# Kernel tuning notes

Measured on AMD Instinct MI355X. Metric: run time of the kernel, lower is better.

Reference implementation:

```python
import jax, jax.numpy as jnp
import numpy as np

DIM = 384
HEADS = 12
WS = (2, 7, 7)
SS = (1, 3, 3)
B, D, H, W = 4, 8, 56, 56
N = WS[0] * WS[1] * WS[2]  # 98


def _win_part_np(x, ws):
    b, d, h, w, c = x.shape
    x = x.reshape(b, d // ws[0], ws[0], h // ws[1], ws[1], w // ws[2], ws[2], c)
    return x.transpose(0, 1, 3, 5, 2, 4, 6, 7).reshape(-1, ws[0] * ws[1] * ws[2], c)


def setup_inputs() -> dict:
    key = jax.random.key(0)
    ks = jax.random.split(key, 6)
    s = 0.02
    x = jax.random.normal(ks[0], (B, D, H, W, DIM), jnp.float32)
    # relative position index (static int buffer)
    coords = np.stack(np.meshgrid(np.arange(WS[0]), np.arange(WS[1]), np.arange(WS[2]), indexing='ij')).reshape(3, -1)
    rel = (coords[:, :, None] - coords[:, None, :]).transpose(1, 2, 0)
    rel[..., 0] += WS[0] - 1
    rel[..., 1] += WS[1] - 1
    rel[..., 2] += WS[2] - 1
    rel[..., 0] *= (2 * WS[1] - 1) * (2 * WS[2] - 1)
    rel[..., 1] *= 2 * WS[2] - 1
    rel_index = jnp.asarray(rel.sum(-1), jnp.int32)  # [N, N]
    # shifted-window attention mask (standard Swin construction)
    img = np.zeros((1, D, H, W, 1), np.float32)
    cnt = 0
    for dsl in (slice(0, -WS[0]), slice(-WS[0], -SS[0]), slice(-SS[0], None)):
        for hsl in (slice(0, -WS[1]), slice(-WS[1], -SS[1]), slice(-SS[1], None)):
            for wsl in (slice(0, -WS[2]), slice(-WS[2], -SS[2]), slice(-SS[2], None)):
                img[:, dsl, hsl, wsl, :] = cnt
                cnt += 1
    mw = _win_part_np(img, WS).squeeze(-1)  # [nW, N]
    attn_mask = np.where(mw[:, None, :] != mw[:, :, None], -100.0, 0.0).astype(np.float32)
    table_size = (2 * WS[0] - 1) * (2 * WS[1] - 1) * (2 * WS[2] - 1)
    return {
        'x': x,
        'mask': jnp.asarray(attn_mask),
        'rel_table': jax.random.normal(ks[1], (table_size, HEADS), jnp.float32) * s,
        'rel_index': rel_index,
        'qkv_w': jax.random.normal(ks[2], (3 * DIM, DIM), jnp.float32) * s,
        'qkv_b': jnp.zeros((3 * DIM,), jnp.float32),
        'proj_w': jax.random.normal(ks[3], (DIM, DIM), jnp.float32) * s,
        'proj_b': jnp.zeros((DIM,), jnp.float32),
        'g1': jnp.ones((DIM,), jnp.float32), 'b1': jnp.zeros((DIM,), jnp.float32),
        'g2': jnp.ones((DIM,), jnp.float32), 'b2': jnp.zeros((DIM,), jnp.float32),
        'fc1_w': jax.random.normal(ks[4], (DIM, DIM), jnp.float32) * s,
        'fc1_b': jnp.zeros((DIM,), jnp.float32),
        'fc2_w': jax.random.normal(ks[5], (DIM, DIM), jnp.float32) * s,
        'fc2_b': jnp.zeros((DIM,), jnp.float32),
    }


def _ln(x, g, b, eps=1e-5):
    mu = x.mean(-1, keepdims=True)
    var = jnp.mean((x - mu) ** 2, axis=-1, keepdims=True)
    return (x - mu) * jax.lax.rsqrt(var + eps) * g + b


def _window_partition(x, ws):
    b, d, h, w, c = x.shape
    x = x.reshape(b, d // ws[0], ws[0], h // ws[1], ws[1], w // ws[2], ws[2], c)
    return x.transpose(0, 1, 3, 5, 2, 4, 6, 7).reshape(-1, ws[0] * ws[1] * ws[2], c)


def _window_reverse(win, ws, b, d, h, w):
    x = win.reshape(b, d // ws[0], h // ws[1], w // ws[2], ws[0], ws[1], ws[2], -1)
    return x.transpose(0, 1, 4, 2, 5, 3, 6, 7).reshape(b, d, h, w, -1)


def reference(x, mask, rel_table, rel_index, qkv_w, qkv_b, proj_w, proj_b,
              g1, b1, g2, b2, fc1_w, fc1_b, fc2_w, fc2_b):
    shortcut = x
    h = _ln(x, g1, b1)
    b, d, hh, ww, c = h.shape
    # get_window_size: clamp window/shift to input extents (static here)
    ws = [min(WS[i], (d, hh, ww)[i]) for i in range(3)]
    ss = [0 if (d, hh, ww)[i] <= WS[i] else SS[i] for i in range(3)]
    pad = [(ws[i] - (d, hh, ww)[i] % ws[i]) % ws[i] for i in range(3)]
    h = jnp.pad(h, ((0, 0), (0, pad[0]), (0, pad[1]), (0, pad[2]), (0, 0)))
    dp, hp, wp = h.shape[1:4]
    if any(ss):
        h = jnp.roll(h, shift=(-ss[0], -ss[1], -ss[2]), axis=(1, 2, 3))
    xw = _window_partition(h, ws)  # [B_, N, C]
    bw, n, _ = xw.shape
    hd = c // HEADS
    qkv = (xw @ qkv_w.T + qkv_b).reshape(bw, n, 3, HEADS, hd).transpose(2, 0, 3, 1, 4)
    q, k, v = qkv[0], qkv[1], qkv[2]  # [B_, H, N, hd]
    scale = hd ** -0.5
    attn = jnp.einsum('bhnd,bhmd->bhnm', q * scale, k)
    bias = rel_table[rel_index[:n, :n].reshape(-1)].reshape(n, n, HEADS).transpose(2, 0, 1)
    attn = attn + bias[None]
    nW = mask.shape[0]
    attn = attn.reshape(bw // nW, nW, HEADS, n, n) + mask[None, :, None]
    attn = jax.nn.softmax(attn.reshape(bw, HEADS, n, n), axis=-1)
    out = jnp.einsum('bhnm,bhmd->bhnd', attn, v).transpose(0, 2, 1, 3).reshape(bw, n, c)
    out = out @ proj_w.T + proj_b
    out = _window_reverse(out, ws, b, dp, hp, wp)
    if any(ss):
        out = jnp.roll(out, shift=(ss[0], ss[1], ss[2]), axis=(1, 2, 3))
    out = out[:, :d, :hh, :ww, :]
    x1 = shortcut + out
    h2 = _ln(x1, g2, b2)
    mlp = jax.nn.gelu(h2 @ fc1_w.T + fc1_b, approximate=False) @ fc2_w.T + fc2_b
    return x1 + mlp
```

## Files before the change

### kernel.cpp

```cpp
#include <hip/hip_runtime.h>
#include <hip/hip_bf16.h>

#define HEADS 12
#define NWIN 1024
#define NW_MASK 256
#define NTOK 98
#define CDIM 384
#define NROWS (NWIN * NTOK)
#define QKVN (3 * CDIM)
#define PSTR 136
#define LOG2E 1.4426950408889634f
#define SCALE_LOG2E 0.25503486f

using u16 = unsigned short;
typedef __attribute__((ext_vector_type(8))) short short8;
typedef __attribute__((ext_vector_type(4))) short s16x4;
typedef __attribute__((ext_vector_type(4))) float f32x4;
typedef __attribute__((ext_vector_type(2))) unsigned u32x2;

__device__ __forceinline__ float b2f(u16 u) { return __uint_as_float(((unsigned)u) << 16); }
__device__ __forceinline__ u16 f2b(float f) {
  unsigned u = __float_as_uint(f);
  u += 0x7FFF + ((u >> 16) & 1);
  return (u16)(u >> 16);
}

__device__ __forceinline__ int tok_of_row(int r) {
  int win = r / NTOK;
  int j   = r - win * NTOK;
  int b   = win >> 8;
  int wl  = win & 255;
  int wd = wl >> 6, wh = (wl >> 3) & 7, ww = wl & 7;
  int od = j / 49; int rem = j - od * 49;
  int oh = rem / 7; int ow = rem - oh * 7;
  int sd = (wd * 2 + od + 1) & 7;
  int sh = wh * 7 + oh + 3; if (sh >= 56) sh -= 56;
  int sw = ww * 7 + ow + 3; if (sw >= 56) sw -= 56;
  return ((b * 8 + sd) * 56 + sh) * 56 + sw;
}

__global__ void detect_kernel(const unsigned* __restrict__ g1w, int* __restrict__ flag) {
  if (threadIdx.x == 0 && blockIdx.x == 0)
    flag[0] = (g1w[0] == 0x3F800000u) ? 1 : 0;
}

__device__ __forceinline__ float raw_at(const void* src, size_t j, int isf32) {
  return isf32 ? ((const float*)src)[j] : b2f(((const u16*)src)[j]);
}

struct CvtArgs {
  const void* src[12];
  unsigned off[13];
};
__global__ __launch_bounds__(256) void cvt_all(CvtArgs a, u16* __restrict__ dst,
                                               const int* __restrict__ flag) {
  int i = blockIdx.x * 256 + threadIdx.x;
  if (i >= (int)a.off[12]) return;
  int s = 0;
#pragma unroll
  for (int k = 1; k < 12; ++k) s += (i >= (int)a.off[k]);
  int j = i - (int)a.off[s];
  dst[i] = flag[0] ? f2b(((const float*)a.src[s])[j]) : ((const u16*)a.src[s])[j];
}

template<bool GATHER>
__global__ __launch_bounds__(256) void ln_kernel(const void* __restrict__ in,
                                                 const u16* __restrict__ gam,
                                                 const u16* __restrict__ bet,
                                                 u16* __restrict__ outp,
                                                 const int* __restrict__ flag,
                                                 int maybe_f32) {
  int wrow = blockIdx.x * 4 + (threadIdx.x >> 6);
  int lane = threadIdx.x & 63;
  int isf32 = maybe_f32 ? flag[0] : 0;
  size_t srow = GATHER ? (size_t)tok_of_row(wrow) : (size_t)wrow;
  const u16*   ip16 = (const u16*)in + srow * CDIM;
  const float* ip32 = (const float*)in + srow * CDIM;
  float xv[6]; float s = 0.f, s2 = 0.f;
#pragma unroll
  for (int i = 0; i < 6; ++i) {
    int c = lane + 64 * i;
    xv[i] = isf32 ? ip32[c] : b2f(ip16[c]);
    s += xv[i]; s2 += xv[i] * xv[i];
  }
#pragma unroll
  for (int off = 1; off < 64; off <<= 1) {
    s  += __shfl_xor(s, off);
    s2 += __shfl_xor(s2, off);
  }
  float mu = s * (1.f / CDIM);
  float var = s2 * (1.f / CDIM) - mu * mu;
  float rstd = rsqrtf(var + 1e-5f);
  u16* op = outp + (size_t)wrow * CDIM;
#pragma unroll
  for (int i = 0; i < 6; ++i) {
    int c = lane + 64 * i;
    op[c] = f2b((xv[i] - mu) * rstd * b2f(gam[c]) + b2f(bet[c]));
  }
}

__global__ void bias_kernel(const void* __restrict__ tab, const int* __restrict__ idx,
                            float* __restrict__ biasf, const int* __restrict__ flag) {
  int i = blockIdx.x * 256 + threadIdx.x;
  if (i >= HEADS * NTOK * 100) return;
  int isf32 = flag[0];
  int h = i / (NTOK * 100);
  int rem = i - h * (NTOK * 100);
  int q = rem / 100, t = rem - q * 100;
  biasf[i] = (t < NTOK) ? raw_at(tab, (size_t)idx[q * NTOK + t] * HEADS + h, isf32) * LOG2E : 0.f;
}

__global__ void maskp_kernel(const void* __restrict__ msrc, u16* __restrict__ mdst,
                             const int* __restrict__ flag) {
  int i = blockIdx.x * 256 + threadIdx.x;
  if (i >= NW_MASK * NTOK * 100) return;
  int isf32 = flag[0];
  int w = i / (NTOK * 100);
  int rem = i - w * (NTOK * 100);
  int q = rem / 100, t = rem - q * 100;
  mdst[i] = (t < NTOK) ? f2b(raw_at(msrc, (size_t)(w * NTOK + q) * NTOK + t, isf32) * LOG2E)
                       : (u16)0;
}

__device__ __forceinline__ void gload16(const u16* g, u16* l) {
  __builtin_amdgcn_global_load_lds((const __attribute__((address_space(1))) unsigned*)g,
                                   (__attribute__((address_space(3))) unsigned*)l,
                                   16, 0, 0);
}

template<int EPI>
__global__ __launch_bounds__(256) void gemm_bt(const u16* __restrict__ A, int lda,
                                               const u16* __restrict__ W,
                                               const u16* __restrict__ bias,
                                               int NB, void* __restrict__ outb, int ldo,
                                               const void* __restrict__ aux,
                                               const int* __restrict__ flag) {
  __shared__ __align__(16) u16 lA[128 * 32];
  __shared__ __align__(16) u16 lB[128 * 32];
  int bid = blockIdx.x;
  int mb = bid / NB, nb = bid - mb * NB;
  int row0 = mb * 128, col0 = nb * 128;
  int tid = threadIdx.x;
  int lane = tid & 63;
  int wid = tid >> 6;
  int wr = (wid >> 1) * 64, wc = (wid & 1) * 64;
  f32x4 zero = {0.f, 0.f, 0.f, 0.f};
  f32x4 acc[4][4];
#pragma unroll
  for (int m = 0; m < 4; ++m)
#pragma unroll
    for (int n = 0; n < 4; ++n) acc[m][n] = zero;

  int e0 = tid * 8;
  int e1 = 2048 + tid * 8;
  int r0 = e0 >> 5, c0 = e0 & 31;
  int r1 = e1 >> 5, c1 = e1 & 31;
  int g = (lane >> 4) * 8, fr = lane & 15;

  for (int kt = 0; kt < CDIM; kt += 32) {
    gload16(&A[(size_t)(row0 + r0) * lda + kt + c0], &lA[e0]);
    gload16(&A[(size_t)(row0 + r1) * lda + kt + c1], &lA[e1]);
    gload16(&W[(size_t)(col0 + r0) * CDIM + kt + c0], &lB[e0]);
    gload16(&W[(size_t)(col0 + r1) * CDIM + kt + c1], &lB[e1]);
    __syncthreads();
    short8 af[4], bf[4];
#pragma unroll
    for (int m = 0; m < 4; ++m) af[m] = *(const short8*)&lA[(wr + m * 16 + fr) * 32 + g];
#pragma unroll
    for (int n = 0; n < 4; ++n) bf[n] = *(const short8*)&lB[(wc + n * 16 + fr) * 32 + g];
#pragma unroll
    for (int m = 0; m < 4; ++m)
#pragma unroll
      for (int n = 0; n < 4; ++n)
        acc[m][n] = __builtin_amdgcn_mfma_f32_16x16x32_bf16(af[m], bf[n], acc[m][n], 0, 0, 0);
    __syncthreads();
  }

  int isf32 = (EPI == 1 || EPI == 3) ? flag[0] : 0;
  int colo = lane & 15;
  int rowo = (lane >> 4) * 4;
  float bv[4];
#pragma unroll
  for (int n = 0; n < 4; ++n) bv[n] = b2f(bias[col0 + wc + n * 16 + colo]);
#pragma unroll
  for (int m = 0; m < 4; ++m) {
#pragma unroll
    for (int r = 0; r < 4; ++r) {
      int gr = row0 + wr + m * 16 + rowo + r;
      int t = (EPI == 1 || EPI == 3) ? tok_of_row(gr) : 0;
#pragma unroll
      for (int n = 0; n < 4; ++n) {
        int gc = col0 + wc + n * 16 + colo;
        float v = acc[m][n][r] + bv[n];
        if (EPI == 0) {
          ((u16*)outb)[(size_t)gr * ldo + gc] = f2b(v);
        } else if (EPI == 1) {
          float xs = isf32 ? ((const float*)aux)[(size_t)t * CDIM + gc]
                           : b2f(((const u16*)aux)[(size_t)t * CDIM + gc]);
          ((u16*)outb)[(size_t)gr * ldo + gc] = f2b(v + xs);
        } else if (EPI == 2) {
          float ge = 0.5f * v * (1.f + erff(v * 0.70710678118654752f));
          ((u16*)outb)[(size_t)gr * ldo + gc] = f2b(ge);
        } else {
          float x1v = b2f(((const u16*)aux)[(size_t)gr * CDIM + gc]);
          float o = v + x1v;
          if (isf32) ((float*)outb)[(size_t)t * CDIM + gc] = o;
          else       ((u16*)outb)[(size_t)t * CDIM + gc] = f2b(o);
        }
      }
    }
  }
}

__global__ __launch_bounds__(256, 3) void attn_mfma(u16* __restrict__ qkv,
                                                    const u16* __restrict__ maskp,
                                                    const float* __restrict__ biasf) {
  __shared__ __align__(16) u16 P4[4][16 * PSTR];
  int wid = threadIdx.x >> 6, lane = threadIdx.x & 63;
  int gh = blockIdx.x * 4 + wid;
  int win = gh / HEADS, hd = gh - win * HEADS;
  int l15 = lane & 15, g = lane >> 4;
  u16* P = P4[wid];
  const size_t base = (size_t)win * NTOK * QKVN + (size_t)hd * 32;
  u16* qp = qkv + base;
  const u16* kp = qkv + base + CDIM;
  const u16* vp = qkv + base + 2 * CDIM;
  const f32x4 zero = {0.f, 0.f, 0.f, 0.f};

  { u32x2 z = {0u, 0u}; *(u32x2*)&P[l15 * PSTR + 112 + 4 * g] = z; }

  short8 kf[7];
#pragma unroll
  for (int n = 0; n < 7; ++n) {
    int tok = n * 16 + l15; if (tok > NTOK - 1) tok = NTOK - 1;
    kf[n] = *(const short8*)&kp[(size_t)tok * QKVN + 8 * g];
  }
  short8 vf[2][4];
#pragma unroll
  for (int kk = 0; kk < 4; ++kk)
#pragma unroll
    for (int i = 0; i < 8; ++i) {
      int tok = 32 * kk + 8 * g + i;
      const u16* vr = vp + (size_t)tok * QKVN + l15;
      u16 v0 = (tok < NTOK) ? vr[0]  : (u16)0;
      u16 v1 = (tok < NTOK) ? vr[16] : (u16)0;
      vf[0][kk][i] = (short)v0;
      vf[1][kk][i] = (short)v1;
    }

  const float* brow = biasf + (size_t)hd * NTOK * 100;
  const u16*   mrow = maskp + (size_t)(win & (NW_MASK - 1)) * NTOK * 100;

  for (int m = 0; m < 7; ++m) {
    int qrow = m * 16 + l15;
    int qr = qrow > NTOK - 1 ? NTOK - 1 : qrow;
    short8 qf = *(const short8*)&qp[(size_t)qr * QKVN + 8 * g];
    f32x4 st[7];
#pragma unroll
    for (int n = 0; n < 7; ++n)
      st[n] = __builtin_amdgcn_mfma_f32_16x16x32_bf16(kf[n], qf, zero, 0, 0, 0);

    float pv[7][4];
    float mx = -1e30f;
#pragma unroll
    for (int n = 0; n < 7; ++n) {
      f32x4 bb = *(const f32x4*)&brow[(size_t)qr * 100 + n * 16 + 4 * g];
      s16x4 mm = *(const s16x4*)&mrow[(size_t)qr * 100 + n * 16 + 4 * g];
#pragma unroll
      for (int r = 0; r < 4; ++r) {
        int tok = n * 16 + 4 * g + r;
        float s = st[n][r] * SCALE_LOG2E + bb[r] + b2f((u16)mm[r]);
        if (tok > NTOK - 1) s = -1e30f;
        pv[n][r] = s;
        mx = fmaxf(mx, s);
      }
    }
    mx = fmaxf(mx, __shfl_xor(mx, 16));
    mx = fmaxf(mx, __shfl_xor(mx, 32));
    float sum = 0.f;
#pragma unroll
    for (int n = 0; n < 7; ++n)
#pragma unroll
      for (int r = 0; r < 4; ++r) {
        float e = exp2f(pv[n][r] - mx);
        pv[n][r] = e; sum += e;
      }
    sum += __shfl_xor(sum, 16);
    sum += __shfl_xor(sum, 32);
    float inv = 1.f / sum;
#pragma unroll
    for (int n = 0; n < 7; ++n) {
      __hip_bfloat162 h0 = __float22bfloat162_rn(make_float2(pv[n][0] * inv, pv[n][1] * inv));
      __hip_bfloat162 h1 = __float22bfloat162_rn(make_float2(pv[n][2] * inv, pv[n][3] * inv));
      u32x2 wv = { *(unsigned*)&h0, *(unsigned*)&h1 };
      *(u32x2*)&P[l15 * PSTR + n * 16 + 4 * g] = wv;
    }
    f32x4 oa0 = zero, oa1 = zero;
#pragma unroll
    for (int kk = 0; kk < 4; ++kk) {
      short8 pf = *(const short8*)&P[l15 * PSTR + kk * 32 + 8 * g];
      oa0 = __builtin_amdgcn_mfma_f32_16x16x32_bf16(pf, vf[0][kk], oa0, 0, 0, 0);
      oa1 = __builtin_amdgcn_mfma_f32_16x16x32_bf16(pf, vf[1][kk], oa1, 0, 0, 0);
    }
#pragma unroll
    for (int r = 0; r < 4; ++r) {
      int row = m * 16 + 4 * g + r;
      if (row < NTOK) {
        qp[(size_t)row * QKVN + l15]      = f2b(oa0[r]);
        qp[(size_t)row * QKVN + 16 + l15] = f2b(oa1[r]);
      }
    }
  }
}

extern "C" void kernel_launch(void* const* d_in, const int* in_sizes, int n_in,
                              void* d_out, int out_size, void* d_ws, size_t ws_size,
                              hipStream_t stream) {
  (void)in_sizes; (void)n_in; (void)out_size; (void)ws_size;
  const void* x    = d_in[0];
  const int* ridx  = (const int*)d_in[3];

  char* ws = (char*)d_ws;
  const size_t SZ_QKV = (size_t)NROWS * QKVN * 2;
  const size_t SZ_MAT = (size_t)NROWS * CDIM * 2;
  const size_t SZ_BIAS = (size_t)HEADS * NTOK * 100 * 4;
  const size_t SZ_MASKP = (size_t)NW_MASK * NTOK * 100 * 2;
  u16* qkv     = (u16*)ws;
  u16* bufA    = (u16*)(ws + SZ_QKV);
  u16* bufX1   = (u16*)(ws + SZ_QKV + SZ_MAT);
  float* biasf = (float*)(ws + SZ_QKV + 2 * SZ_MAT);
  u16* maskp   = (u16*)(ws + SZ_QKV + 2 * SZ_MAT + SZ_BIAS);
  int* flag    = (int*)(ws + SZ_QKV + 2 * SZ_MAT + SZ_BIAS + SZ_MASKP);
  u16* cvt     = (u16*)((char*)flag + 256);

  detect_kernel<<<1, 64, 0, stream>>>((const unsigned*)d_in[8], flag);

  CvtArgs ca;
  unsigned off = 0;
  u16* cp[16];
  for (int k = 0; k < 12; ++k) {
    int i = 4 + k;
    ca.src[k] = d_in[i];
    ca.off[k] = off;
    cp[i] = cvt + off;
    off += (unsigned)in_sizes[i];
  }
  ca.off[12] = off;
  cvt_all<<<(off + 255) / 256, 256, 0, stream>>>(ca, cvt, flag);

  bias_kernel<<<(HEADS * NTOK * 100 + 255) / 256, 256, 0, stream>>>(d_in[2], ridx, biasf, flag);
  maskp_kernel<<<(NW_MASK * NTOK * 100 + 255) / 256, 256, 0, stream>>>(d_in[1], maskp, flag);
  ln_kernel<true><<<NROWS / 4, 256, 0, stream>>>(x, cp[8], cp[9], bufA, flag, 1);
  gemm_bt<0><<<(NROWS / 128) * (QKVN / 128), 256, 0, stream>>>(
      bufA, CDIM, cp[4], cp[5], QKVN / 128, qkv, QKVN, nullptr, flag);
  attn_mfma<<<(NWIN * HEADS) / 4, 256, 0, stream>>>(qkv, maskp, biasf);
  gemm_bt<1><<<(NROWS / 128) * (CDIM / 128), 256, 0, stream>>>(
      qkv, QKVN, cp[6], cp[7], CDIM / 128, bufX1, CDIM, x, flag);
  ln_kernel<false><<<NROWS / 4, 256, 0, stream>>>(bufX1, cp[10], cp[11], bufA, flag, 0);
  u16* fc1out = qkv;
  gemm_bt<2><<<(NROWS / 128) * (CDIM / 128), 256, 0, stream>>>(
      bufA, CDIM, cp[12], cp[13], CDIM / 128, fc1out, CDIM, nullptr, flag);
  gemm_bt<3><<<(NROWS / 128) * (CDIM / 128), 256, 0, stream>>>(
      fc1out, CDIM, cp[14], cp[15], CDIM / 128, d_out, CDIM, bufX1, flag);
}
```

Before: 804.0 us.

## Fuse LN2+fc1+GELU+fc2 into one MLP kernel, merge prep kernels, swizzle QKV GEMM

New measurement: 1.077 ms. +34.0%, slower.

```diff
diff --git a/kernel.cpp b/kernel.cpp
--- a/kernel.cpp
+++ b/kernel.cpp
@@ -11,6 +11,9 @@
 #define PSTR 136
 #define LOG2E 1.4426950408889634f
 #define SCALE_LOG2E 0.25503486f
+#define KSTEPS 12
+#define MTOK 64
+#define XNS 400
 
 using u16 = unsigned short;
 typedef __attribute__((ext_vector_type(8))) short short8;
@@ -39,6 +42,12 @@
   return ((b * 8 + sd) * 56 + sh) * 56 + sw;
 }
 
+__device__ __forceinline__ int xcd_swz(int bid, int nwg) {
+  int q = nwg >> 3, r = nwg & 7;
+  int xcd = bid & 7, i = bid >> 3;
+  return ((xcd < r) ? xcd * (q + 1) : r * (q + 1) + (xcd - r) * q) + i;
+}
+
 __global__ void detect_kernel(const unsigned* __restrict__ g1w, int* __restrict__ flag) {
   if (threadIdx.x == 0 && blockIdx.x == 0)
     flag[0] = (g1w[0] == 0x3F800000u) ? 1 : 0;
@@ -63,17 +72,15 @@
   dst[i] = flag[0] ? f2b(((const float*)a.src[s])[j]) : ((const u16*)a.src[s])[j];
 }
 
-template<bool GATHER>
 __global__ __launch_bounds__(256) void ln_kernel(const void* __restrict__ in,
                                                  const u16* __restrict__ gam,
                                                  const u16* __restrict__ bet,
                                                  u16* __restrict__ outp,
-                                                 const int* __restrict__ flag,
-                                                 int maybe_f32) {
+                                                 const int* __restrict__ flag) {
   int wrow = blockIdx.x * 4 + (threadIdx.x >> 6);
   int lane = threadIdx.x & 63;
-  int isf32 = maybe_f32 ? flag[0] : 0;
-  size_t srow = GATHER ? (size_t)tok_of_row(wrow) : (size_t)wrow;
+  int isf32 = flag[0];
+  size_t srow = (size_t)tok_of_row(wrow);
   const u16*   ip16 = (const u16*)in + srow * CDIM;
   const float* ip32 = (const float*)in + srow * CDIM;
   float xv[6]; float s = 0.f, s2 = 0.f;
@@ -99,22 +106,18 @@
   }
 }
 
-__global__ void bias_kernel(const void* __restrict__ tab, const int* __restrict__ idx,
+__global__ void prep_kernel(const void* __restrict__ msrc, u16* __restrict__ mdst,
+                            const void* __restrict__ tab, const int* __restrict__ idx,
                             float* __restrict__ biasf, const int* __restrict__ flag) {
   int i = blockIdx.x * 256 + threadIdx.x;
-  if (i >= HEADS * NTOK * 100) return;
   int isf32 = flag[0];
-  int h = i / (NTOK * 100);
-  int rem = i - h * (NTOK * 100);
-  int q = rem / 100, t = rem - q * 100;
-  biasf[i] = (t < NTOK) ? raw_at(tab, (size_t)idx[q * NTOK + t] * HEADS + h, isf32) * LOG2E : 0.f;
-}
-
-__global__ void maskp_kernel(const void* __restrict__ msrc, u16* __restrict__ mdst,
-                             const int* __restrict__ flag) {
-  int i = blockIdx.x * 256 + threadIdx.x;
+  if (i < HEADS * NTOK * 100) {
+    int h = i / (NTOK * 100);
+    int rem = i - h * (NTOK * 100);
+    int q = rem / 100, t = rem - q * 100;
+    biasf[i] = (t < NTOK) ? raw_at(tab, (size_t)idx[q * NTOK + t] * HEADS + h, isf32) * LOG2E : 0.f;
+  }
   if (i >= NW_MASK * NTOK * 100) return;
-  int isf32 = flag[0];
   int w = i / (NTOK * 100);
   int rem = i - w * (NTOK * 100);
   int q = rem / 100, t = rem - q * 100;
@@ -128,7 +131,7 @@
                                    16, 0, 0);
 }
 
-template<int EPI>
+template<int EPI, bool SWZ>
 __global__ __launch_bounds__(256) void gemm_bt(const u16* __restrict__ A, int lda,
                                                const u16* __restrict__ W,
                                                const u16* __restrict__ bias,
@@ -137,7 +140,7 @@
                                                const int* __restrict__ flag) {
   __shared__ __align__(16) u16 lA[128 * 32];
   __shared__ __align__(16) u16 lB[128 * 32];
-  int bid = blockIdx.x;
+  int bid = SWZ ? xcd_swz(blockIdx.x, gridDim.x) : blockIdx.x;
   int mb = bid / NB, nb = bid - mb * NB;
   int row0 = mb * 128, col0 = nb * 128;
   int tid = threadIdx.x;
@@ -176,7 +179,7 @@
     __syncthreads();
   }
 
-  int isf32 = (EPI == 1 || EPI == 3) ? flag[0] : 0;
+  int isf32 = (EPI == 1) ? flag[0] : 0;
   int colo = lane & 15;
   int rowo = (lane >> 4) * 4;
   float bv[4];
@@ -187,32 +190,25 @@
 #pragma unroll
     for (int r = 0; r < 4; ++r) {
       int gr = row0 + wr + m * 16 + rowo + r;
-      int t = (EPI == 1 || EPI == 3) ? tok_of_row(gr) : 0;
+      int t = (EPI == 1) ? tok_of_row(gr) : 0;
 #pragma unroll
       for (int n = 0; n < 4; ++n) {
         int gc = col0 + wc + n * 16 + colo;
         float v = acc[m][n][r] + bv[n];
         if (EPI == 0) {
           ((u16*)outb)[(size_t)gr * ldo + gc] = f2b(v);
-        } else if (EPI == 1) {
+        } else {
           float xs = isf32 ? ((const float*)aux)[(size_t)t * CDIM + gc]
                            : b2f(((const u16*)aux)[(size_t)t * CDIM + gc]);
           ((u16*)outb)[(size_t)gr * ldo + gc] = f2b(v + xs);
-        } else if (EPI == 2) {
-          float ge = 0.5f * v * (1.f + erff(v * 0.70710678118654752f));
-          ((u16*)outb)[(size_t)gr * ldo + gc] = f2b(ge);
-        } else {
-          float x1v = b2f(((const u16*)aux)[(size_t)gr * CDIM + gc]);
-          float o = v + x1v;
-          if (isf32) ((float*)outb)[(size_t)t * CDIM + gc] = o;
-          else       ((u16*)outb)[(size_t)t * CDIM + gc] = f2b(o);
         }
       }
     }
   }
 }
 
-__global__ __launch_bounds__(256, 3) void attn_mfma(u16* __restrict__ qkv,
+__global__ __launch_bounds__(256, 3) void attn_mfma(const u16* __restrict__ qkv,
+                                                    u16* __restrict__ obuf,
                                                     const u16* __restrict__ maskp,
                                                     const float* __restrict__ biasf) {
   __shared__ __align__(16) u16 P4[4][16 * PSTR];
@@ -222,9 +218,10 @@
   int l15 = lane & 15, g = lane >> 4;
   u16* P = P4[wid];
   const size_t base = (size_t)win * NTOK * QKVN + (size_t)hd * 32;
-  u16* qp = qkv + base;
+  const u16* qp = qkv + base;
   const u16* kp = qkv + base + CDIM;
   const u16* vp = qkv + base + 2 * CDIM;
+  u16* op = obuf + (size_t)win * NTOK * CDIM + hd * 32;
   const f32x4 zero = {0.f, 0.f, 0.f, 0.f};
 
   { u32x2 z = {0u, 0u}; *(u32x2*)&P[l15 * PSTR + 112 + 4 * g] = z; }
@@ -306,9 +303,119 @@
     for (int r = 0; r < 4; ++r) {
       int row = m * 16 + 4 * g + r;
       if (row < NTOK) {
-        qp[(size_t)row * QKVN + l15]      = f2b(oa0[r]);
-        qp[(size_t)row * QKVN + 16 + l15] = f2b(oa1[r]);
+        op[(size_t)row * CDIM + l15]      = f2b(oa0[r]);
+        op[(size_t)row * CDIM + 16 + l15] = f2b(oa1[r]);
       }
+    }
+  }
+}
+
+__global__ __launch_bounds__(512, 3) void mlp_fused(const u16* __restrict__ x1,
+                                                    const u16* __restrict__ gam,
+                                                    const u16* __restrict__ bet,
+                                                    const u16* __restrict__ w1,
+                                                    const u16* __restrict__ b1v,
+                                                    const u16* __restrict__ w2,
+                                                    const u16* __restrict__ b2v,
+                                                    void* __restrict__ outp,
+                                                    const int* __restrict__ flag) {
+  __shared__ __align__(16) u16 xn[MTOK * XNS];
+  int tid = threadIdx.x, lane = tid & 63, wid = tid >> 6;
+  int fr = lane & 15, gq = lane >> 4;
+  int rgrp = wid >> 1, cgrp = wid & 1;
+  int row0 = blockIdx.x * MTOK;
+  const f32x4 zero = {0.f, 0.f, 0.f, 0.f};
+
+  {
+    int row = tid >> 3, q = tid & 7;
+    const u16* ip = x1 + (size_t)(row0 + row) * CDIM + q * 48;
+    short8 xv[6]; float s = 0.f, s2 = 0.f;
+#pragma unroll
+    for (int i = 0; i < 6; ++i) {
+      xv[i] = *(const short8*)&ip[i * 8];
+#pragma unroll
+      for (int e = 0; e < 8; ++e) { float f = b2f((u16)xv[i][e]); s += f; s2 += f * f; }
+    }
+    s += __shfl_xor(s, 1); s2 += __shfl_xor(s2, 1);
+    s += __shfl_xor(s, 2); s2 += __shfl_xor(s2, 2);
+    s += __shfl_xor(s, 4); s2 += __shfl_xor(s2, 4);
+    float mu = s * (1.f / CDIM);
+    float var = s2 * (1.f / CDIM) - mu * mu;
+    float rstd = rsqrtf(var + 1e-5f);
+    u16* op = &xn[row * XNS + q * 48];
+#pragma unroll
+    for (int i = 0; i < 6; ++i) {
+      short8 o;
+#pragma unroll
+      for (int e = 0; e < 8; ++e) {
+        int c = q * 48 + i * 8 + e;
+        o[e] = (short)f2b((b2f((u16)xv[i][e]) - mu) * rstd * b2f(gam[c]) + b2f(bet[c]));
+      }
+      *(short8*)&op[i * 8] = o;
+    }
+  }
+  __syncthreads();
+
+  short8 af[KSTEPS];
+#pragma unroll
+  for (int kk = 0; kk < KSTEPS; ++kk)
+    af[kk] = *(const short8*)&xn[(rgrp * 16 + fr) * XNS + kk * 32 + 8 * gq];
+
+  f32x4 acc[12];
+#pragma unroll
+  for (int n = 0; n < 12; ++n) acc[n] = zero;
+
+#pragma unroll
+  for (int n = 0; n < 12; ++n) {
+    int c = cgrp * 192 + n * 16 + fr;
+    const u16* wrow = w1 + (size_t)c * CDIM + 8 * gq;
+#pragma unroll
+    for (int kk = 0; kk < KSTEPS; ++kk) {
+      short8 bf = *(const short8*)&wrow[kk * 32];
+      acc[n] = __builtin_amdgcn_mfma_f32_16x16x32_bf16(af[kk], bf, acc[n], 0, 0, 0);
+    }
+  }
+
+#pragma unroll
+  for (int n = 0; n < 12; ++n) {
+    int c = cgrp * 192 + n * 16 + fr;
+    float bb = b2f(b1v[c]);
+#pragma unroll
+    for (int r = 0; r < 4; ++r) {
+      float v = acc[n][r] + bb;
+      float ge = 0.5f * v * (1.f + erff(v * 0.70710678118654752f));
+      xn[(rgrp * 16 + gq * 4 + r) * XNS + c] = f2b(ge);
+      acc[n][r] = 0.f;
+    }
+  }
+  __syncthreads();
+
+#pragma unroll
+  for (int kk = 0; kk < KSTEPS; ++kk)
+    af[kk] = *(const short8*)&xn[(rgrp * 16 + fr) * XNS + kk * 32 + 8 * gq];
+
+#pragma unroll
+  for (int n = 0; n < 12; ++n) {
+    int c = cgrp * 192 + n * 16 + fr;
+    const u16* wrow = w2 + (size_t)c * CDIM + 8 * gq;
+#pragma unroll
+    for (int kk = 0; kk < KSTEPS; ++kk) {
+      short8 bf = *(const short8*)&wrow[kk * 32];
+      acc[n] = __builtin_amdgcn_mfma_f32_16x16x32_bf16(af[kk], bf, acc[n], 0, 0, 0);
+    }
+  }
+
+  int isf32 = flag[0];
+#pragma unroll
+  for (int r = 0; r < 4; ++r) {
+    int grow = row0 + rgrp * 16 + gq * 4 + r;
+    int t = tok_of_row(grow);
+#pragma unroll
+    for (int n = 0; n < 12; ++n) {
+      int c = cgrp * 192 + n * 16 + fr;
+      float o = acc[n][r] + b2f(b2v[c]) + b2f(x1[(size_t)grow * CDIM + c]);
+      if (isf32) ((float*)outp)[(size_t)t * CDIM + c] = o;
+      else       ((u16*)outp)[(size_t)t * CDIM + c] = f2b(o);
     }
   }
 }
@@ -316,7 +423,7 @@
 extern "C" void kernel_launch(void* const* d_in, const int* in_sizes, int n_in,
                               void* d_out, int out_size, void* d_ws, size_t ws_size,
                               hipStream_t stream) {
-  (void)in_sizes; (void)n_in; (void)out_size; (void)ws_size;
+  (void)n_in; (void)out_size; (void)ws_size;
   const void* x    = d_in[0];
   const int* ridx  = (const int*)d_in[3];
 
@@ -348,18 +455,14 @@
   ca.off[12] = off;
   cvt_all<<<(off + 255) / 256, 256, 0, stream>>>(ca, cvt, flag);
 
-  bias_kernel<<<(HEADS * NTOK * 100 + 255) / 256, 256, 0, stream>>>(d_in[2], ridx, biasf, flag);
-  maskp_kernel<<<(NW_MASK * NTOK * 100 + 255) / 256, 256, 0, stream>>>(d_in[1], maskp, flag);
-  ln_kernel<true><<<NROWS / 4, 256, 0, stream>>>(x, cp[8], cp[9], bufA, flag, 1);
-  gemm_bt<0><<<(NROWS / 128) * (QKVN / 128), 256, 0, stream>>>(
+  prep_kernel<<<(NW_MASK * NTOK * 100 + 255) / 256, 256, 0, stream>>>(
+      d_in[1], maskp, d_in[2], ridx, biasf, flag);
+  ln_kernel<<<NROWS / 4, 256, 0, stream>>>(x, cp[8], cp[9], bufA, flag);
+  gemm_bt<0, true><<<(NROWS / 128) * (QKVN / 128), 256, 0, stream>>>(
       bufA, CDIM, cp[4], cp[5], QKVN / 128, qkv, QKVN, nullptr, flag);
-  attn_mfma<<<(NWIN * HEADS) / 4, 256, 0, stream>>>(qkv, maskp, biasf);
-  gemm_bt<1><<<(NROWS / 128) * (CDIM / 128), 256, 0, stream>>>(
-      qkv, QKVN, cp[6], cp[7], CDIM / 128, bufX1, CDIM, x, flag);
-  ln_kernel<false><<<NROWS / 4, 256, 0, stream>>>(bufX1, cp[10], cp[11], bufA, flag, 0);
-  u16* fc1out = qkv;
-  gemm_bt<2><<<(NROWS / 128) * (CDIM / 128), 256, 0, stream>>>(
-      bufA, CDIM, cp[12], cp[13], CDIM / 128, fc1out, CDIM, nullptr, flag);
-  gemm_bt<3><<<(NROWS / 128) * (CDIM / 128), 256, 0, stream>>>(
-      fc1out, CDIM, cp[14], cp[15], CDIM / 128, d_out, CDIM, bufX1, flag);
-}
+  attn_mfma<<<(NWIN * HEADS) / 4, 256, 0, stream>>>(qkv, bufA, maskp, biasf);
+  gemm_bt<1, false><<<(NROWS / 128) * (CDIM / 128), 256, 0, stream>>>(
+      bufA, CDIM, cp[6], cp[7], CDIM / 128, bufX1, CDIM, x, flag);
+  mlp_fused<<<NROWS / MTOK, 512, 0, stream>>>(
+      bufX1, cp[10], cp[11], cp[12], cp[13], cp[14], cp[15], d_out, flag);
+}
```
